# Kernel optimization log

Measured on AMD Instinct MI355X. Metric: run time of the kernel, lower is better.

## Reference

```python
import jax, jax.numpy as jnp
import numpy as np

LN_EPS = 1e-5

def layernorm(x, g, b):
    mu = jnp.mean(x, axis=-1, keepdims=True)
    var = jnp.mean(jnp.square(x - mu), axis=-1, keepdims=True)
    return (x - mu) * jax.lax.rsqrt(var + LN_EPS) * g + b

def setup_inputs() -> dict:
    B, T, C, H = 4, 1024, 1024, 16
    hd = C // H
    key = jax.random.key(0)
    ks = jax.random.split(key, 16)
    s = 0.02
    inp = {
        "x":  jax.random.normal(ks[0], (B, T, C), jnp.float32),
        # per-head QKV projections, stacked over heads: [H, C, hd] / [H, hd]
        "Wq": jax.random.normal(ks[1], (H, C, hd), jnp.float32) * s,
        "bq": jax.random.normal(ks[2], (H, hd), jnp.float32) * s,
        "Wk": jax.random.normal(ks[3], (H, C, hd), jnp.float32) * s,
        "bk": jax.random.normal(ks[4], (H, hd), jnp.float32) * s,
        "Wv": jax.random.normal(ks[5], (H, C, hd), jnp.float32) * s,
        "bv": jax.random.normal(ks[6], (H, hd), jnp.float32) * s,
        # LayerNorm params: ln1, ln2 (decoder), lnf (inside FeedForward)
        "g1": 1.0 + jax.random.normal(ks[7], (C,), jnp.float32) * s,
        "b1": jax.random.normal(ks[8], (C,), jnp.float32) * s,
        "g2": 1.0 + jax.random.normal(ks[9], (C,), jnp.float32) * s,
        "b2": jax.random.normal(ks[10], (C,), jnp.float32) * s,
        "gf": 1.0 + jax.random.normal(ks[11], (C,), jnp.float32) * s,
        "bf": jax.random.normal(ks[12], (C,), jnp.float32) * s,
        # FFN
        "W1": jax.random.normal(ks[13], (C, 4 * C), jnp.float32) * s,
        "b1f": jnp.zeros((4 * C,), jnp.float32),
        "W2": jax.random.normal(ks[14], (4 * C, C), jnp.float32) * s,
        "b2f": jnp.zeros((C,), jnp.float32),
    }
    return inp

def reference(x, Wq, bq, Wk, bk, Wv, bv, g1, b1, g2, b2, gf, bf, W1, b1f, W2, b2f):
    B, T, C = x.shape
    h = layernorm(x, g1, b1)                      # ln1
    # multi-head causal attention (per-head projections stacked on H)
    q = jnp.einsum("btc,hcd->bhtd", h, Wq) + bq[None, :, None, :]
    k = jnp.einsum("btc,hcd->bhtd", h, Wk) + bk[None, :, None, :]
    v = jnp.einsum("btc,hcd->bhtd", h, Wv) + bv[None, :, None, :]
    # NOTE: original scales by C**-0.5 (n_embd), not head_size**-0.5
    att = jnp.einsum("bhtd,bhsd->bhts", q, k) / jnp.sqrt(jnp.float32(C))
    causal = jnp.tril(jnp.ones((T, T), bool))
    att = jnp.where(causal, att, -jnp.inf)
    att = jax.nn.softmax(att, axis=-1)
    o = jnp.einsum("bhts,bhsd->bhtd", att, v)     # [B,H,T,hd]
    o = jnp.transpose(o, (0, 2, 1, 3)).reshape(B, T, C)  # concat heads
    x2 = h + o
    x3 = layernorm(x2, g2, b2)                    # ln2
    # FeedForward: hf = ln(x3); out = net(hf) + hf  (residual uses post-LN!)
    hf = layernorm(x3, gf, bf)
    ff = jax.nn.relu(hf @ W1 + b1f) @ W2 + b2f + hf
    return x3 + ff                                # dropout is identity in eval
```

## Files before the change

### kernel.cpp

```cpp
#include <hip/hip_runtime.h>
#include <hip/hip_bf16.h>


typedef __attribute__((ext_vector_type(8))) short short8;
typedef __attribute__((ext_vector_type(4))) short short4v;
typedef __attribute__((ext_vector_type(4))) float f32x4;

#define DEVI static __device__ __forceinline__

#define BAR() __builtin_amdgcn_s_barrier()
#define SB0() __builtin_amdgcn_sched_barrier(0)
#define LGKM0()                                         \
  {                                                     \
    asm volatile("s_waitcnt lgkmcnt(0)" ::: "memory");  \
    __builtin_amdgcn_sched_barrier(0);                  \
  }
#define VMW(n)                                              \
  {                                                         \
    asm volatile("s_waitcnt vmcnt(" #n ")" ::: "memory");   \
    __builtin_amdgcn_sched_barrier(0);                      \
  }

DEVI void gload_lds16(const void* g, void* l) {
  __builtin_amdgcn_global_load_lds(
      (const __attribute__((address_space(1))) void*)g,
      (__attribute__((address_space(3))) void*)l, 16, 0, 0);
}

DEVI float bf2f(short s) {
  union { float f; unsigned u; } cv;
  cv.u = ((unsigned)(unsigned short)s) << 16;
  return cv.f;
}
DEVI short f2bf(float f) {
  union { float f; unsigned u; } cv;
  cv.f = f;
  unsigned u = cv.u;
  u += 0x7FFFu + ((u >> 16) & 1u);
  return (short)(u >> 16);
}

DEVI void block_reduce2(float& s, float& s2, float* red, int t) {
#pragma unroll
  for (int off = 1; off < 64; off <<= 1) {
    s += __shfl_xor(s, off, 64);
    s2 += __shfl_xor(s2, off, 64);
  }
  __syncthreads();
  if ((t & 63) == 0) { red[(t >> 6) * 2] = s; red[(t >> 6) * 2 + 1] = s2; }
  __syncthreads();
  s = red[0] + red[2] + red[4] + red[6];
  s2 = red[1] + red[3] + red[5] + red[7];
}

DEVI void xcd_swz(int gx, int gy, int& bx, int& by) {
  const int flat = blockIdx.y * gx + blockIdx.x;
  const int c = (gx * gy) >> 3;
  const int nf = (flat & 7) * c + (flat >> 3);
  bx = nf % gx;
  by = nf / gx;
}

__global__ __launch_bounds__(256) void transpose_to_bf16(
    const float* __restrict__ in, short* __restrict__ out, int R, int C) {
  __shared__ float tile[32][33];
  const int b = blockIdx.z;
  in += (size_t)b * R * C;
  out += (size_t)b * R * C;
  const int r0 = blockIdx.y * 32, c0 = blockIdx.x * 32;
  const int tx = threadIdx.x, ty = threadIdx.y;
#pragma unroll
  for (int i = 0; i < 32; i += 8)
    tile[ty + i][tx] = in[(size_t)(r0 + ty + i) * C + c0 + tx];
  __syncthreads();
#pragma unroll
  for (int i = 0; i < 32; i += 8)
    out[(size_t)(c0 + ty + i) * R + r0 + tx] = f2bf(tile[tx][ty + i]);
}

__global__ __launch_bounds__(256) void transpose_qkv(
    const float* __restrict__ Wq, const float* __restrict__ Wk,
    const float* __restrict__ Wv, short* __restrict__ out) {
  __shared__ float tile[32][33];
  const int z = blockIdx.z;
  const int sel = z >> 4, b = z & 15;
  const float* in = (sel == 0) ? Wq : (sel == 1) ? Wk : Wv;
  in += (size_t)b * 1024 * 64;
  short* o = out + (size_t)sel * 1024 * 1024 + (size_t)b * 1024 * 64;
  const int r0 = blockIdx.y * 32, c0 = blockIdx.x * 32;
  const int tx = threadIdx.x, ty = threadIdx.y;
#pragma unroll
  for (int i = 0; i < 32; i += 8)
    tile[ty + i][tx] = in[(size_t)(r0 + ty + i) * 64 + c0 + tx];
  __syncthreads();
#pragma unroll
  for (int i = 0; i < 32; i += 8)
    o[(size_t)(c0 + ty + i) * 1024 + r0 + tx] = f2bf(tile[tx][ty + i]);
}

__global__ __launch_bounds__(256) void ln1_kernel(
    const float* __restrict__ x, const float* __restrict__ g,
    const float* __restrict__ b, float* __restrict__ hf,
    short* __restrict__ hb) {
  __shared__ float red[8];
  const int row = blockIdx.x, t = threadIdx.x;
  float4 v = ((const float4*)(x + (size_t)row * 1024))[t];
  float s = v.x + v.y + v.z + v.w;
  float s2 = v.x * v.x + v.y * v.y + v.z * v.z + v.w * v.w;
  block_reduce2(s, s2, red, t);
  const float mu = s * (1.0f / 1024.0f);
  const float rstd = rsqrtf(s2 * (1.0f / 1024.0f) - mu * mu + 1e-5f);
  float4 gv = ((const float4*)g)[t], bv = ((const float4*)b)[t];
  float4 o;
  o.x = (v.x - mu) * rstd * gv.x + bv.x;
  o.y = (v.y - mu) * rstd * gv.y + bv.y;
  o.z = (v.z - mu) * rstd * gv.z + bv.z;
  o.w = (v.w - mu) * rstd * gv.w + bv.w;
  ((float4*)(hf + (size_t)row * 1024))[t] = o;
  short4v p = {f2bf(o.x), f2bf(o.y), f2bf(o.z), f2bf(o.w)};
  ((short4v*)(hb + (size_t)row * 1024))[t] = p;
}

__global__ __launch_bounds__(256) void ln2f_kernel(
    const float* __restrict__ h, const float* __restrict__ o,
    const float* __restrict__ g2, const float* __restrict__ b2,
    const float* __restrict__ gf, const float* __restrict__ bfp,
    float* __restrict__ x3, short* __restrict__ hfb) {
  __shared__ float red[8];
  const int row = blockIdx.x, t = threadIdx.x;
  float4 hv = ((const float4*)(h + (size_t)row * 1024))[t];
  float4 ov = ((const float4*)(o + (size_t)row * 1024))[t];
  float4 v;
  v.x = hv.x + ov.x; v.y = hv.y + ov.y; v.z = hv.z + ov.z; v.w = hv.w + ov.w;
  float s = v.x + v.y + v.z + v.w;
  float s2 = v.x * v.x + v.y * v.y + v.z * v.z + v.w * v.w;
  block_reduce2(s, s2, red, t);
  float mu = s * (1.0f / 1024.0f);
  float rstd = rsqrtf(s2 * (1.0f / 1024.0f) - mu * mu + 1e-5f);
  float4 gv = ((const float4*)g2)[t], bv = ((const float4*)b2)[t];
  float4 xv;
  xv.x = (v.x - mu) * rstd * gv.x + bv.x;
  xv.y = (v.y - mu) * rstd * gv.y + bv.y;
  xv.z = (v.z - mu) * rstd * gv.z + bv.z;
  xv.w = (v.w - mu) * rstd * gv.w + bv.w;
  ((float4*)(x3 + (size_t)row * 1024))[t] = xv;
  s = xv.x + xv.y + xv.z + xv.w;
  s2 = xv.x * xv.x + xv.y * xv.y + xv.z * xv.z + xv.w * xv.w;
  block_reduce2(s, s2, red, t);
  mu = s * (1.0f / 1024.0f);
  rstd = rsqrtf(s2 * (1.0f / 1024.0f) - mu * mu + 1e-5f);
  float4 gv2 = ((const float4*)gf)[t], bv2 = ((const float4*)bfp)[t];
  short4v pk = {f2bf((xv.x - mu) * rstd * gv2.x + bv2.x),
                f2bf((xv.y - mu) * rstd * gv2.y + bv2.y),
                f2bf((xv.z - mu) * rstd * gv2.z + bv2.z),
                f2bf((xv.w - mu) * rstd * gv2.w + bv2.w)};
  ((short4v*)(hfb + (size_t)row * 1024))[t] = pk;
}

template <int EPI>
DEVI void gemm8_body(const short* __restrict__ A, const short* __restrict__ B,
                     int K, int kbase, int m0, int n0,
                     const float* __restrict__ f0, const float* __restrict__ f1,
                     const float* __restrict__ f2, short* __restrict__ s0,
                     short* __restrict__ s1, short* __restrict__ s2,
                     float* __restrict__ fo) {
  extern __shared__ __align__(16) char lds[];
  constexpr int NT = 16;
  const int tid = threadIdx.x;
  const int l = tid & 63, w = tid >> 6;
  const int wrM = w >> 2, wcN = w & 3;
  const int lr = l & 15, lg = l >> 4;

  const int cswz = (((lr & 1) << 2) | lg) ^ (lr >> 1);
  const int laneoff = ((lr >> 1) << 7) + (cswz << 4);

  const int rsel = l >> 3;
  const int scz = (l & 7) ^ rsel;
  const int s_roff = w * 16 + rsel * 2 + (scz >> 2);
  const int s_kc = (scz & 3) * 8;
  const short* Asrc = A + (size_t)(m0 + s_roff) * K + kbase + s_kc;
  const short* Bsrc = B + (size_t)(n0 + s_roff) * K + kbase + s_kc;
  const size_t rstep = (size_t)128 * K;

  auto STAGE = [&](int op, int kh, int t) {
    const short* g = (op ? Bsrc : Asrc) + t * 64 + kh * 32;
    char* d = lds + ((t & 1) * 65536 + op * 32768 + kh * 16384 + w * 1024);
    gload_lds16(g, d);
    gload_lds16(g + rstep, d + 8192);
  };

  f32x4 acc[8][4] = {};

  STAGE(0, 0, 0); STAGE(1, 0, 0); STAGE(0, 1, 0); STAGE(1, 1, 0);
  VMW(4); BAR(); SB0();

  for (int t = 0; t < NT; ++t) {
    const char* pa = lds + (t & 1) * 65536 + wrM * 8192 + laneoff;
    const char* pb = lds + (t & 1) * 65536 + 32768 + wcN * 4096 + laneoff;
    const bool st = (t + 1) < NT;
    short8 a[8], b[4];

#pragma unroll
    for (int mt = 0; mt < 8; ++mt) a[mt] = *(const short8*)(pa + mt * 1024);
#pragma unroll
    for (int nt = 0; nt < 4; ++nt) b[nt] = *(const short8*)(pb + nt * 1024);
    if (st) STAGE(0, 0, t + 1);
    BAR(); LGKM0();
    __builtin_amdgcn_s_setprio(1);
#pragma unroll
    for (int mt = 0; mt < 8; ++mt) {
      acc[mt][0] = __builtin_amdgcn_mfma_f32_16x16x32_bf16(a[mt], b[0], acc[mt][0], 0, 0, 0);
      acc[mt][1] = __builtin_amdgcn_mfma_f32_16x16x32_bf16(a[mt], b[1], acc[mt][1], 0, 0, 0);
    }
    __builtin_amdgcn_s_setprio(0);
    BAR(); SB0();

    if (st) STAGE(1, 0, t + 1);
    BAR(); SB0();
    __builtin_amdgcn_s_setprio(1);
#pragma unroll
    for (int mt = 0; mt < 8; ++mt) {
      acc[mt][2] = __builtin_amdgcn_mfma_f32_16x16x32_bf16(a[mt], b[2], acc[mt][2], 0, 0, 0);
      acc[mt][3] = __builtin_amdgcn_mfma_f32_16x16x32_bf16(a[mt], b[3], acc[mt][3], 0, 0, 0);
    }
    __builtin_amdgcn_s_setprio(0);
    if (st) { VMW(4); } else { VMW(0); }
    BAR(); SB0();

    pa += 16384; pb += 16384;
#pragma unroll
    for (int mt = 0; mt < 8; ++mt) a[mt] = *(const short8*)(pa + mt * 1024);
#pragma unroll
    for (int nt = 0; nt < 4; ++nt) b[nt] = *(const short8*)(pb + nt * 1024);
    if (st) STAGE(0, 1, t + 1);
    BAR(); LGKM0();
    __builtin_amdgcn_s_setprio(1);
#pragma unroll
    for (int mt = 0; mt < 8; ++mt) {
      acc[mt][0] = __builtin_amdgcn_mfma_f32_16x16x32_bf16(a[mt], b[0], acc[mt][0], 0, 0, 0);
      acc[mt][1] = __builtin_amdgcn_mfma_f32_16x16x32_bf16(a[mt], b[1], acc[mt][1], 0, 0, 0);
    }
    __builtin_amdgcn_s_setprio(0);
    BAR(); SB0();

    if (st) STAGE(1, 1, t + 1);
    BAR(); SB0();
    __builtin_amdgcn_s_setprio(1);
#pragma unroll
    for (int mt = 0; mt < 8; ++mt) {
      acc[mt][2] = __builtin_amdgcn_mfma_f32_16x16x32_bf16(a[mt], b[2], acc[mt][2], 0, 0, 0);
      acc[mt][3] = __builtin_amdgcn_mfma_f32_16x16x32_bf16(a[mt], b[3], acc[mt][3], 0, 0, 0);
    }
    __builtin_amdgcn_s_setprio(0);
    if (st) VMW(4);
    BAR(); SB0();
  }

#pragma unroll
  for (int mt = 0; mt < 8; ++mt) {
#pragma unroll
    for (int nt = 0; nt < 4; ++nt) {
      const int col = n0 + wcN * 64 + nt * 16 + lr;
      const int row0 = m0 + wrM * 128 + mt * 16 + lg * 4;
      if constexpr (EPI == 0) {
        const int sel = col >> 10, nn = col & 1023;
        const int hh = nn >> 6, dd = nn & 63;
        const int bb = row0 >> 10, tt0 = row0 & 1023;
        if (sel == 2) {
          const float bias = f2[nn];
          short4v pk = {f2bf(acc[mt][nt][0] + bias), f2bf(acc[mt][nt][1] + bias),
                        f2bf(acc[mt][nt][2] + bias), f2bf(acc[mt][nt][3] + bias)};
          *(short4v*)&s2[(((size_t)(bb * 16 + hh)) * 64 + dd) * 1024 + tt0] = pk;
        } else {
          const float bias = (sel == 0) ? f0[nn] : f1[nn];
          short* dst = (sel == 0) ? s0 : s1;
#pragma unroll
          for (int r = 0; r < 4; ++r)
            dst[(((size_t)(bb * 16 + hh)) * 1024 + tt0 + r) * 64 + dd] =
                f2bf(acc[mt][nt][r] + bias);
        }
      } else if constexpr (EPI == 1) {
#pragma unroll
        for (int r = 0; r < 4; ++r) {
          float val = fmaxf(acc[mt][nt][r] + f0[col], 0.0f);
          s0[(size_t)(row0 + r) * 4096 + col] = f2bf(val);
        }
      } else {
#pragma unroll
        for (int r = 0; r < 4; ++r)
          fo[(size_t)(row0 + r) * 1024 + col] = acc[mt][nt][r];
      }
    }
  }
}

__global__ __launch_bounds__(512, 2) void gemm8_qkv(
    const short* __restrict__ A, const short* __restrict__ B,
    const float* __restrict__ bq, const float* __restrict__ bk,
    const float* __restrict__ bv, short* __restrict__ q,
    short* __restrict__ k, short* __restrict__ vt) {
  int bx, by;
  xcd_swz(12, 16, bx, by);
  gemm8_body<0>(A, B, 1024, 0, by * 256, bx * 256, bq, bk, bv,
                q, k, vt, nullptr);
}

__global__ __launch_bounds__(512, 2) void gemm8_ffn1(
    const short* __restrict__ A, const short* __restrict__ B,
    const float* __restrict__ b1f, short* __restrict__ u) {
  int bx, by;
  xcd_swz(16, 16, bx, by);
  gemm8_body<1>(A, B, 1024, 0, by * 256, bx * 256, b1f,
                nullptr, nullptr, u, nullptr, nullptr, nullptr);
}

__global__ __launch_bounds__(512, 2) void gemm8_ffn2sk(
    const short* __restrict__ A, const short* __restrict__ B,
    float* __restrict__ part) {
  const int z = blockIdx.z;
  int bx, by;
  xcd_swz(4, 16, bx, by);
  gemm8_body<2>(A, B, 4096, z * 1024, by * 256, bx * 256,
                nullptr, nullptr, nullptr, nullptr, nullptr, nullptr,
                part + (size_t)z * 4096 * 1024);
}

__global__ __launch_bounds__(256) void ffn2_reduce(
    const float* __restrict__ part, const float* __restrict__ b2f,
    const short* __restrict__ hfb, const float* __restrict__ x3,
    float* __restrict__ out) {
  const size_t i = (size_t)blockIdx.x * 256 + threadIdx.x;
  const size_t S = (size_t)4096 * 1024 / 4;
  float4 a0 = ((const float4*)part)[i];
  float4 a1 = ((const float4*)part)[i + S];
  float4 a2 = ((const float4*)part)[i + 2 * S];
  float4 a3 = ((const float4*)part)[i + 3 * S];
  float4 bb = ((const float4*)b2f)[i & 255];
  float4 xv = ((const float4*)x3)[i];
  short4v hv = ((const short4v*)hfb)[i];
  float4 o;
  o.x = a0.x + a1.x + a2.x + a3.x + bb.x + bf2f(hv.x) + xv.x;
  o.y = a0.y + a1.y + a2.y + a3.y + bb.y + bf2f(hv.y) + xv.y;
  o.z = a0.z + a1.z + a2.z + a3.z + bb.z + bf2f(hv.z) + xv.z;
  o.w = a0.w + a1.w + a2.w + a3.w + bb.w + bf2f(hv.w) + xv.w;
  ((float4*)out)[i] = o;
}

__global__ __launch_bounds__(256, 5) void attn_kernel(
    const short* __restrict__ q, const short* __restrict__ k,
    const short* __restrict__ vt, float* __restrict__ o) {
  __shared__ __align__(16) short Ksm[64 * 64];
  __shared__ __align__(16) short Vsm[64 * 64];
  __shared__ __align__(16) short Psm[4 * 16 * 64];
  const int bh = blockIdx.x;
  const int qt = 15 - blockIdx.y;
  const int tid = threadIdx.x, lane = tid & 63, w = tid >> 6;
  const int lr = lane & 15, lg = lane >> 4;

  const short* qb = q + (size_t)bh * 1024 * 64;
  const short* kb = k + (size_t)bh * 1024 * 64;
  const short* vb = vt + (size_t)bh * 64 * 1024;

  const int qrow = qt * 64 + w * 16 + lr;
  short8 qf0 = *(const short8*)&qb[(size_t)qrow * 64 + lg * 8];
  short8 qf1 = *(const short8*)&qb[(size_t)qrow * 64 + 32 + lg * 8];

  f32x4 oacc[4] = {};
  float mrun = -1e30f, lrun = 0.0f;

  const float scale2 = 0.03125f * 1.44269504088896f;
  const int srow = tid >> 3;
  const int sc8 = tid & 7;
  char* pw = (char*)(Psm + w * 1024);
  const int qloc = w * 16 + lr;
  const int rowswz = (lr & 7) << 4;

  short8 kreg[2], vreg[2];
#pragma unroll
  for (int p = 0; p < 2; ++p) {
    const int rr = srow + p * 32;
    kreg[p] = *(const short8*)&kb[(size_t)rr * 64 + sc8 * 8];
    vreg[p] = *(const short8*)&vb[(size_t)rr * 1024 + sc8 * 8];
  }

  for (int kt = 0; kt <= qt; ++kt) {
#pragma unroll
    for (int p = 0; p < 2; ++p) {
      const int rr = srow + p * 32;
      *(short8*)((char*)Ksm + rr * 128 + ((sc8 ^ (rr & 7)) << 4)) = kreg[p];
      *(short8*)((char*)Vsm + rr * 128 + ((sc8 ^ (rr & 7)) << 4)) = vreg[p];
    }
    __syncthreads();
    if (kt < qt) {
#pragma unroll
      for (int p = 0; p < 2; ++p) {
        const int rr = srow + p * 32;
        kreg[p] =
            *(const short8*)&kb[((size_t)((kt + 1) * 64 + rr)) * 64 + sc8 * 8];
        vreg[p] =
            *(const short8*)&vb[(size_t)rr * 1024 + (kt + 1) * 64 + sc8 * 8];
      }
    }

    f32x4 sfr[4];
#pragma unroll
    for (int nt = 0; nt < 4; ++nt) {
      const int krow = nt * 16 + lr;
      short8 kf0 = *(const short8*)((const char*)Ksm + krow * 128 +
                                    (((0 + lg) ^ (krow & 7)) << 4));
      short8 kf1 = *(const short8*)((const char*)Ksm + krow * 128 +
                                    (((4 + lg) ^ (krow & 7)) << 4));
      f32x4 z = {};
      z = __builtin_amdgcn_mfma_f32_16x16x32_bf16(kf0, qf0, z, 0, 0, 0);
      z = __builtin_amdgcn_mfma_f32_16x16x32_bf16(kf1, qf1, z, 0, 0, 0);
      sfr[nt] = z;
    }
    if (kt == qt) {
#pragma unroll
      for (int nt = 0; nt < 4; ++nt) {
        const int kb0 = nt * 16 + lg * 4;
#pragma unroll
        for (int r = 0; r < 4; ++r)
          sfr[nt][r] = (kb0 + r <= qloc) ? sfr[nt][r] * scale2 : -1e30f;
      }
    } else {
#pragma unroll
      for (int nt = 0; nt < 4; ++nt)
#pragma unroll
        for (int r = 0; r < 4; ++r) sfr[nt][r] *= scale2;
    }
    float pm;
    {
      float a0 = fmaxf(fmaxf(sfr[0][0], sfr[0][1]), fmaxf(sfr[0][2], sfr[0][3]));
      float a1 = fmaxf(fmaxf(sfr[1][0], sfr[1][1]), fmaxf(sfr[1][2], sfr[1][3]));
      float a2 = fmaxf(fmaxf(sfr[2][0], sfr[2][1]), fmaxf(sfr[2][2], sfr[2][3]));
      float a3 = fmaxf(fmaxf(sfr[3][0], sfr[3][1]), fmaxf(sfr[3][2], sfr[3][3]));
      pm = fmaxf(fmaxf(a0, a1), fmaxf(a2, a3));
      pm = fmaxf(pm, __shfl_xor(pm, 16, 64));
      pm = fmaxf(pm, __shfl_xor(pm, 32, 64));
    }
    if (!__all(pm - mrun <= 8.0f)) {
      const float mnew = fmaxf(mrun, pm);
      const float alpha = exp2f(mrun - mnew);
      mrun = mnew;
      lrun *= alpha;
#pragma unroll
      for (int nt = 0; nt < 4; ++nt)
#pragma unroll
        for (int r = 0; r < 4; ++r) oacc[nt][r] *= alpha;
    }
    float rs;
    {
#pragma unroll
      for (int nt = 0; nt < 4; ++nt)
#pragma unroll
        for (int r = 0; r < 4; ++r) sfr[nt][r] = exp2f(sfr[nt][r] - mrun);
      float s0 = (sfr[0][0] + sfr[0][1]) + (sfr[0][2] + sfr[0][3]);
      float s1 = (sfr[1][0] + sfr[1][1]) + (sfr[1][2] + sfr[1][3]);
      float s2 = (sfr[2][0] + sfr[2][1]) + (sfr[2][2] + sfr[2][3]);
      float s3 = (sfr[3][0] + sfr[3][1]) + (sfr[3][2] + sfr[3][3]);
      rs = (s0 + s1) + (s2 + s3);
      rs += __shfl_xor(rs, 16, 64);
      rs += __shfl_xor(rs, 32, 64);
    }
    lrun += rs;

#pragma unroll
    for (int nt = 0; nt < 4; ++nt) {
      unsigned w0, w1;
      asm("v_cvt_pk_bf16_f32 %0, %1, %2"
          : "=v"(w0) : "v"(sfr[nt][0]), "v"(sfr[nt][1]));
      asm("v_cvt_pk_bf16_f32 %0, %1, %2"
          : "=v"(w1) : "v"(sfr[nt][2]), "v"(sfr[nt][3]));
      uint2 pk2 = {w0, w1};
      *(uint2*)(pw + lr * 128 + ((nt * 32 + lg * 8) ^ rowswz)) = pk2;
    }

#pragma unroll
    for (int kc = 0; kc < 2; ++kc) {
      short8 pb8 = *(const short8*)(pw + lr * 128 + ((kc * 64 + lg * 16) ^ rowswz));
#pragma unroll
      for (int nt = 0; nt < 4; ++nt) {
        const int vrow = nt * 16 + lr;
        short8 vf = *(const short8*)((const char*)Vsm + vrow * 128 +
                                     (((kc * 4 + lg) ^ (vrow & 7)) << 4));
        oacc[nt] = __builtin_amdgcn_mfma_f32_16x16x32_bf16(vf, pb8, oacc[nt], 0, 0, 0);
      }
    }
    __syncthreads();
  }

  const float inv = 1.0f / lrun;
  float* ob = o + (size_t)(bh >> 4) * 1024 * 1024 +
              (size_t)(qt * 64 + qloc) * 1024 + (bh & 15) * 64;
#pragma unroll
  for (int nt = 0; nt < 4; ++nt) {
    float4 ov = {oacc[nt][0] * inv, oacc[nt][1] * inv, oacc[nt][2] * inv,
                 oacc[nt][3] * inv};
    *(float4*)&ob[nt * 16 + lg * 4] = ov;
  }
}

extern "C" void kernel_launch(void* const* d_in, const int* in_sizes, int n_in,
                              void* d_out, int out_size, void* d_ws,
                              size_t ws_size, hipStream_t stream) {
  const float* x = (const float*)d_in[0];
  const float* Wq = (const float*)d_in[1];
  const float* bq = (const float*)d_in[2];
  const float* Wk = (const float*)d_in[3];
  const float* bk = (const float*)d_in[4];
  const float* Wv = (const float*)d_in[5];
  const float* bv = (const float*)d_in[6];
  const float* g1 = (const float*)d_in[7];
  const float* b1 = (const float*)d_in[8];
  const float* g2 = (const float*)d_in[9];
  const float* b2 = (const float*)d_in[10];
  const float* gf = (const float*)d_in[11];
  const float* bfp = (const float*)d_in[12];
  const float* W1 = (const float*)d_in[13];
  const float* b1f = (const float*)d_in[14];
  const float* W2 = (const float*)d_in[15];
  const float* b2f = (const float*)d_in[16];
  float* out = (float*)d_out;

  hipFuncSetAttribute((const void*)gemm8_qkv,
                      hipFuncAttributeMaxDynamicSharedMemorySize, 131072);
  hipFuncSetAttribute((const void*)gemm8_ffn1,
                      hipFuncAttributeMaxDynamicSharedMemorySize, 131072);
  hipFuncSetAttribute((const void*)gemm8_ffn2sk,
                      hipFuncAttributeMaxDynamicSharedMemorySize, 131072);

  const size_t MB = 1024 * 1024;
  char* p = (char*)d_ws;
  float* hbuf = (float*)(p + 0 * MB);
  short* qbuf = (short*)(p + 16 * MB);
  short* kbuf = (short*)(p + 24 * MB);
  short* vtb = (short*)(p + 32 * MB);
  float* obuf = (float*)(p + 40 * MB);
  short* wqkv_t = (short*)(p + 56 * MB);
  short* w1_t = (short*)(p + 62 * MB);
  float* part = (float*)(p + 0 * MB);
  char* q = p + 70 * MB;
  short* w2_t = (short*)(q + 0 * MB);
  short* hbb = (short*)(q + 8 * MB);
  float* x3b = (float*)(q + 16 * MB);
  short* hfb = (short*)(q + 32 * MB);
  short* ub = (short*)(q + 40 * MB);

  dim3 tb(32, 8);
  transpose_qkv<<<dim3(2, 32, 48), tb, 0, stream>>>(Wq, Wk, Wv, wqkv_t);
  transpose_to_bf16<<<dim3(128, 32, 1), tb, 0, stream>>>(W1, w1_t, 1024, 4096);
  transpose_to_bf16<<<dim3(32, 128, 1), tb, 0, stream>>>(W2, w2_t, 4096, 1024);

  ln1_kernel<<<4096, 256, 0, stream>>>(x, g1, b1, hbuf, hbb);

  gemm8_qkv<<<dim3(12, 16), 512, 131072, stream>>>(hbb, wqkv_t, bq, bk, bv,
                                                   qbuf, kbuf, vtb);

  attn_kernel<<<dim3(64, 16), 256, 0, stream>>>(qbuf, kbuf, vtb, obuf);

  ln2f_kernel<<<4096, 256, 0, stream>>>(hbuf, obuf, g2, b2, gf, bfp, x3b, hfb);

  gemm8_ffn1<<<dim3(16, 16), 512, 131072, stream>>>(hfb, w1_t, b1f, ub);

  gemm8_ffn2sk<<<dim3(4, 16, 4), 512, 131072, stream>>>(ub, w2_t, part);

  ffn2_reduce<<<4096, 256, 0, stream>>>(part, b2f, hfb, x3b, out);
}
```

Baseline: 195.9 us.

## Shrink GEMM tiles to 128x128 with 4 waves and halve split-K

```diff
diff --git a/kernel.cpp b/kernel.cpp
--- a/kernel.cpp
+++ b/kernel.cpp
@@ -158,17 +158,16 @@
 }
 
 template <int EPI>
-DEVI void gemm8_body(const short* __restrict__ A, const short* __restrict__ B,
-                     int K, int kbase, int m0, int n0,
+DEVI void gemm4_body(const short* __restrict__ A, const short* __restrict__ B,
+                     int K, int kbase, int ktiles, int m0, int n0,
                      const float* __restrict__ f0, const float* __restrict__ f1,
                      const float* __restrict__ f2, short* __restrict__ s0,
                      short* __restrict__ s1, short* __restrict__ s2,
                      float* __restrict__ fo) {
   extern __shared__ __align__(16) char lds[];
-  constexpr int NT = 16;
   const int tid = threadIdx.x;
   const int l = tid & 63, w = tid >> 6;
-  const int wrM = w >> 2, wcN = w & 3;
+  const int wrM = w >> 1, wcN = w & 1;
   const int lr = l & 15, lg = l >> 4;
 
   const int cswz = (((lr & 1) << 2) | lg) ^ (lr >> 1);
@@ -180,88 +179,53 @@
   const int s_kc = (scz & 3) * 8;
   const short* Asrc = A + (size_t)(m0 + s_roff) * K + kbase + s_kc;
   const short* Bsrc = B + (size_t)(n0 + s_roff) * K + kbase + s_kc;
-  const size_t rstep = (size_t)128 * K;
+  const size_t rstep = (size_t)64 * K;
 
   auto STAGE = [&](int op, int kh, int t) {
     const short* g = (op ? Bsrc : Asrc) + t * 64 + kh * 32;
-    char* d = lds + ((t & 1) * 65536 + op * 32768 + kh * 16384 + w * 1024);
+    char* d = lds + ((t & 1) * 32768 + op * 16384 + kh * 8192 + w * 1024);
     gload_lds16(g, d);
-    gload_lds16(g + rstep, d + 8192);
+    gload_lds16(g + rstep, d + 4096);
   };
 
-  f32x4 acc[8][4] = {};
+  f32x4 acc[4][4] = {};
 
   STAGE(0, 0, 0); STAGE(1, 0, 0); STAGE(0, 1, 0); STAGE(1, 1, 0);
   VMW(4); BAR(); SB0();
 
-  for (int t = 0; t < NT; ++t) {
-    const char* pa = lds + (t & 1) * 65536 + wrM * 8192 + laneoff;
-    const char* pb = lds + (t & 1) * 65536 + 32768 + wcN * 4096 + laneoff;
-    const bool st = (t + 1) < NT;
-    short8 a[8], b[4];
-
-#pragma unroll
-    for (int mt = 0; mt < 8; ++mt) a[mt] = *(const short8*)(pa + mt * 1024);
-#pragma unroll
-    for (int nt = 0; nt < 4; ++nt) b[nt] = *(const short8*)(pb + nt * 1024);
-    if (st) STAGE(0, 0, t + 1);
-    BAR(); LGKM0();
-    __builtin_amdgcn_s_setprio(1);
-#pragma unroll
-    for (int mt = 0; mt < 8; ++mt) {
-      acc[mt][0] = __builtin_amdgcn_mfma_f32_16x16x32_bf16(a[mt], b[0], acc[mt][0], 0, 0, 0);
-      acc[mt][1] = __builtin_amdgcn_mfma_f32_16x16x32_bf16(a[mt], b[1], acc[mt][1], 0, 0, 0);
-    }
-    __builtin_amdgcn_s_setprio(0);
-    BAR(); SB0();
-
-    if (st) STAGE(1, 0, t + 1);
-    BAR(); SB0();
-    __builtin_amdgcn_s_setprio(1);
-#pragma unroll
-    for (int mt = 0; mt < 8; ++mt) {
-      acc[mt][2] = __builtin_amdgcn_mfma_f32_16x16x32_bf16(a[mt], b[2], acc[mt][2], 0, 0, 0);
-      acc[mt][3] = __builtin_amdgcn_mfma_f32_16x16x32_bf16(a[mt], b[3], acc[mt][3], 0, 0, 0);
-    }
-    __builtin_amdgcn_s_setprio(0);
-    if (st) { VMW(4); } else { VMW(0); }
-    BAR(); SB0();
-
-    pa += 16384; pb += 16384;
-#pragma unroll
-    for (int mt = 0; mt < 8; ++mt) a[mt] = *(const short8*)(pa + mt * 1024);
-#pragma unroll
-    for (int nt = 0; nt < 4; ++nt) b[nt] = *(const short8*)(pb + nt * 1024);
-    if (st) STAGE(0, 1, t + 1);
-    BAR(); LGKM0();
-    __builtin_amdgcn_s_setprio(1);
-#pragma unroll
-    for (int mt = 0; mt < 8; ++mt) {
-      acc[mt][0] = __builtin_amdgcn_mfma_f32_16x16x32_bf16(a[mt], b[0], acc[mt][0], 0, 0, 0);
-      acc[mt][1] = __builtin_amdgcn_mfma_f32_16x16x32_bf16(a[mt], b[1], acc[mt][1], 0, 0, 0);
-    }
-    __builtin_amdgcn_s_setprio(0);
-    BAR(); SB0();
-
-    if (st) STAGE(1, 1, t + 1);
-    BAR(); SB0();
-    __builtin_amdgcn_s_setprio(1);
-#pragma unroll
-    for (int mt = 0; mt < 8; ++mt) {
-      acc[mt][2] = __builtin_amdgcn_mfma_f32_16x16x32_bf16(a[mt], b[2], acc[mt][2], 0, 0, 0);
-      acc[mt][3] = __builtin_amdgcn_mfma_f32_16x16x32_bf16(a[mt], b[3], acc[mt][3], 0, 0, 0);
-    }
-    __builtin_amdgcn_s_setprio(0);
-    if (st) VMW(4);
-    BAR(); SB0();
-  }
-
-#pragma unroll
-  for (int mt = 0; mt < 8; ++mt) {
+  for (int t = 0; t < ktiles; ++t) {
+    const bool st = (t + 1) < ktiles;
+#pragma unroll
+    for (int kh = 0; kh < 2; ++kh) {
+      const char* pa = lds + (t & 1) * 32768 + kh * 8192 + wrM * 4096 + laneoff;
+      const char* pb =
+          lds + (t & 1) * 32768 + 16384 + kh * 8192 + wcN * 4096 + laneoff;
+      short8 a[4], b[4];
+#pragma unroll
+      for (int mt = 0; mt < 4; ++mt) a[mt] = *(const short8*)(pa + mt * 1024);
+#pragma unroll
+      for (int nt = 0; nt < 4; ++nt) b[nt] = *(const short8*)(pb + nt * 1024);
+      if (st) { STAGE(0, kh, t + 1); STAGE(1, kh, t + 1); }
+      LGKM0();
+      __builtin_amdgcn_s_setprio(1);
+#pragma unroll
+      for (int mt = 0; mt < 4; ++mt)
+#pragma unroll
+        for (int nt = 0; nt < 4; ++nt)
+          acc[mt][nt] = __builtin_amdgcn_mfma_f32_16x16x32_bf16(
+              a[mt], b[nt], acc[mt][nt], 0, 0, 0);
+      __builtin_amdgcn_s_setprio(0);
+      if (st) { VMW(4); } else if (kh == 0) { VMW(0); }
+      BAR(); SB0();
+    }
+  }
+
+#pragma unroll
+  for (int mt = 0; mt < 4; ++mt) {
 #pragma unroll
     for (int nt = 0; nt < 4; ++nt) {
       const int col = n0 + wcN * 64 + nt * 16 + lr;
-      const int row0 = m0 + wrM * 128 + mt * 16 + lg * 4;
+      const int row0 = m0 + wrM * 64 + mt * 16 + lg * 4;
       if constexpr (EPI == 0) {
         const int sel = col >> 10, nn = col & 1023;
         const int hh = nn >> 6, dd = nn & 63;
@@ -294,34 +258,34 @@
   }
 }
 
-__global__ __launch_bounds__(512, 2) void gemm8_qkv(
+__global__ __launch_bounds__(256, 2) void gemm4_qkv(
     const short* __restrict__ A, const short* __restrict__ B,
     const float* __restrict__ bq, const float* __restrict__ bk,
     const float* __restrict__ bv, short* __restrict__ q,
     short* __restrict__ k, short* __restrict__ vt) {
   int bx, by;
-  xcd_swz(12, 16, bx, by);
-  gemm8_body<0>(A, B, 1024, 0, by * 256, bx * 256, bq, bk, bv,
-                q, k, vt, nullptr);
-}
-
-__global__ __launch_bounds__(512, 2) void gemm8_ffn1(
+  xcd_swz(24, 32, bx, by);
+  gemm4_body<0>(A, B, 1024, 0, 16, by * 128, bx * 128, bq, bk, bv, q, k, vt,
+                nullptr);
+}
+
+__global__ __launch_bounds__(256, 2) void gemm4_ffn1(
     const short* __restrict__ A, const short* __restrict__ B,
     const float* __restrict__ b1f, short* __restrict__ u) {
   int bx, by;
-  xcd_swz(16, 16, bx, by);
-  gemm8_body<1>(A, B, 1024, 0, by * 256, bx * 256, b1f,
-                nullptr, nullptr, u, nullptr, nullptr, nullptr);
-}
-
-__global__ __launch_bounds__(512, 2) void gemm8_ffn2sk(
+  xcd_swz(32, 32, bx, by);
+  gemm4_body<1>(A, B, 1024, 0, 16, by * 128, bx * 128, b1f, nullptr, nullptr,
+                u, nullptr, nullptr, nullptr);
+}
+
+__global__ __launch_bounds__(256, 2) void gemm4_ffn2sk(
     const short* __restrict__ A, const short* __restrict__ B,
     float* __restrict__ part) {
   const int z = blockIdx.z;
   int bx, by;
-  xcd_swz(4, 16, bx, by);
-  gemm8_body<2>(A, B, 4096, z * 1024, by * 256, bx * 256,
-                nullptr, nullptr, nullptr, nullptr, nullptr, nullptr,
+  xcd_swz(8, 32, bx, by);
+  gemm4_body<2>(A, B, 4096, z * 2048, 32, by * 128, bx * 128, nullptr, nullptr,
+                nullptr, nullptr, nullptr, nullptr,
                 part + (size_t)z * 4096 * 1024);
 }
 
@@ -333,16 +297,14 @@
   const size_t S = (size_t)4096 * 1024 / 4;
   float4 a0 = ((const float4*)part)[i];
   float4 a1 = ((const float4*)part)[i + S];
-  float4 a2 = ((const float4*)part)[i + 2 * S];
-  float4 a3 = ((const float4*)part)[i + 3 * S];
   float4 bb = ((const float4*)b2f)[i & 255];
   float4 xv = ((const float4*)x3)[i];
   short4v hv = ((const short4v*)hfb)[i];
   float4 o;
-  o.x = a0.x + a1.x + a2.x + a3.x + bb.x + bf2f(hv.x) + xv.x;
-  o.y = a0.y + a1.y + a2.y + a3.y + bb.y + bf2f(hv.y) + xv.y;
-  o.z = a0.z + a1.z + a2.z + a3.z + bb.z + bf2f(hv.z) + xv.z;
-  o.w = a0.w + a1.w + a2.w + a3.w + bb.w + bf2f(hv.w) + xv.w;
+  o.x = a0.x + a1.x + bb.x + bf2f(hv.x) + xv.x;
+  o.y = a0.y + a1.y + bb.y + bf2f(hv.y) + xv.y;
+  o.z = a0.z + a1.z + bb.z + bf2f(hv.z) + xv.z;
+  o.w = a0.w + a1.w + bb.w + bf2f(hv.w) + xv.w;
   ((float4*)out)[i] = o;
 }
 
@@ -523,12 +485,12 @@
   const float* b2f = (const float*)d_in[16];
   float* out = (float*)d_out;
 
-  hipFuncSetAttribute((const void*)gemm8_qkv,
-                      hipFuncAttributeMaxDynamicSharedMemorySize, 131072);
-  hipFuncSetAttribute((const void*)gemm8_ffn1,
-                      hipFuncAttributeMaxDynamicSharedMemorySize, 131072);
-  hipFuncSetAttribute((const void*)gemm8_ffn2sk,
-                      hipFuncAttributeMaxDynamicSharedMemorySize, 131072);
+  hipFuncSetAttribute((const void*)gemm4_qkv,
+                      hipFuncAttributeMaxDynamicSharedMemorySize, 65536);
+  hipFuncSetAttribute((const void*)gemm4_ffn1,
+                      hipFuncAttributeMaxDynamicSharedMemorySize, 65536);
+  hipFuncSetAttribute((const void*)gemm4_ffn2sk,
+                      hipFuncAttributeMaxDynamicSharedMemorySize, 65536);
 
   const size_t MB = 1024 * 1024;
   char* p = (char*)d_ws;
@@ -554,16 +516,16 @@
 
   ln1_kernel<<<4096, 256, 0, stream>>>(x, g1, b1, hbuf, hbb);
 
-  gemm8_qkv<<<dim3(12, 16), 512, 131072, stream>>>(hbb, wqkv_t, bq, bk, bv,
-                                                   qbuf, kbuf, vtb);
+  gemm4_qkv<<<dim3(24, 32), 256, 65536, stream>>>(hbb, wqkv_t, bq, bk, bv,
+                                                  qbuf, kbuf, vtb);
 
   attn_kernel<<<dim3(64, 16), 256, 0, stream>>>(qbuf, kbuf, vtb, obuf);
 
   ln2f_kernel<<<4096, 256, 0, stream>>>(hbuf, obuf, g2, b2, gf, bfp, x3b, hfb);
 
-  gemm8_ffn1<<<dim3(16, 16), 512, 131072, stream>>>(hfb, w1_t, b1f, ub);
-
-  gemm8_ffn2sk<<<dim3(4, 16, 4), 512, 131072, stream>>>(ub, w2_t, part);
+  gemm4_ffn1<<<dim3(32, 32), 256, 65536, stream>>>(hfb, w1_t, b1f, ub);
+
+  gemm4_ffn2sk<<<dim3(8, 32, 2), 256, 65536, stream>>>(ub, w2_t, part);
 
   ffn2_reduce<<<4096, 256, 0, stream>>>(part, b2f, hfb, x3b, out);
 }
```

Result: slower. 199.9 us (+2.1%).

## Deepen GEMM LDS pipeline to four 32-wide K stages with prefetch distance three

Applied to the files above, without the earlier changes.

```diff
diff --git a/kernel.cpp b/kernel.cpp
--- a/kernel.cpp
+++ b/kernel.cpp
@@ -165,7 +165,7 @@
                      short* __restrict__ s1, short* __restrict__ s2,
                      float* __restrict__ fo) {
   extern __shared__ __align__(16) char lds[];
-  constexpr int NT = 16;
+  constexpr int NT = 32;
   const int tid = threadIdx.x;
   const int l = tid & 63, w = tid >> 6;
   const int wrM = w >> 2, wcN = w & 3;
@@ -182,29 +182,30 @@
   const short* Bsrc = B + (size_t)(n0 + s_roff) * K + kbase + s_kc;
   const size_t rstep = (size_t)128 * K;
 
-  auto STAGE = [&](int op, int kh, int t) {
-    const short* g = (op ? Bsrc : Asrc) + t * 64 + kh * 32;
-    char* d = lds + ((t & 1) * 65536 + op * 32768 + kh * 16384 + w * 1024);
+  auto STAGE = [&](int op, int t) {
+    const short* g = (op ? Bsrc : Asrc) + t * 32;
+    char* d = lds + ((t & 3) * 32768 + op * 16384 + w * 1024);
     gload_lds16(g, d);
     gload_lds16(g + rstep, d + 8192);
   };
 
   f32x4 acc[8][4] = {};
 
-  STAGE(0, 0, 0); STAGE(1, 0, 0); STAGE(0, 1, 0); STAGE(1, 1, 0);
-  VMW(4); BAR(); SB0();
+  STAGE(0, 0); STAGE(1, 0); STAGE(0, 1); STAGE(1, 1); STAGE(0, 2); STAGE(1, 2);
+  VMW(8); BAR(); SB0();
 
   for (int t = 0; t < NT; ++t) {
-    const char* pa = lds + (t & 1) * 65536 + wrM * 8192 + laneoff;
-    const char* pb = lds + (t & 1) * 65536 + 32768 + wcN * 4096 + laneoff;
-    const bool st = (t + 1) < NT;
+    const char* base = lds + (t & 3) * 32768;
+    const char* pa = base + wrM * 8192 + laneoff;
+    const char* pb = base + 16384 + wcN * 4096 + laneoff;
+    const bool st = (t + 3) < NT;
     short8 a[8], b[4];
 
 #pragma unroll
     for (int mt = 0; mt < 8; ++mt) a[mt] = *(const short8*)(pa + mt * 1024);
-#pragma unroll
-    for (int nt = 0; nt < 4; ++nt) b[nt] = *(const short8*)(pb + nt * 1024);
-    if (st) STAGE(0, 0, t + 1);
+    b[0] = *(const short8*)(pb);
+    b[1] = *(const short8*)(pb + 1024);
+    if (st) STAGE(0, t + 3);
     BAR(); LGKM0();
     __builtin_amdgcn_s_setprio(1);
 #pragma unroll
@@ -215,8 +216,10 @@
     __builtin_amdgcn_s_setprio(0);
     BAR(); SB0();
 
-    if (st) STAGE(1, 0, t + 1);
-    BAR(); SB0();
+    b[2] = *(const short8*)(pb + 2048);
+    b[3] = *(const short8*)(pb + 3072);
+    if (st) STAGE(1, t + 3);
+    BAR(); LGKM0();
     __builtin_amdgcn_s_setprio(1);
 #pragma unroll
     for (int mt = 0; mt < 8; ++mt) {
@@ -224,35 +227,9 @@
       acc[mt][3] = __builtin_amdgcn_mfma_f32_16x16x32_bf16(a[mt], b[3], acc[mt][3], 0, 0, 0);
     }
     __builtin_amdgcn_s_setprio(0);
-    if (st) { VMW(4); } else { VMW(0); }
-    BAR(); SB0();
-
-    pa += 16384; pb += 16384;
-#pragma unroll
-    for (int mt = 0; mt < 8; ++mt) a[mt] = *(const short8*)(pa + mt * 1024);
-#pragma unroll
-    for (int nt = 0; nt < 4; ++nt) b[nt] = *(const short8*)(pb + nt * 1024);
-    if (st) STAGE(0, 1, t + 1);
-    BAR(); LGKM0();
-    __builtin_amdgcn_s_setprio(1);
-#pragma unroll
-    for (int mt = 0; mt < 8; ++mt) {
-      acc[mt][0] = __builtin_amdgcn_mfma_f32_16x16x32_bf16(a[mt], b[0], acc[mt][0], 0, 0, 0);
-      acc[mt][1] = __builtin_amdgcn_mfma_f32_16x16x32_bf16(a[mt], b[1], acc[mt][1], 0, 0, 0);
-    }
-    __builtin_amdgcn_s_setprio(0);
-    BAR(); SB0();
-
-    if (st) STAGE(1, 1, t + 1);
-    BAR(); SB0();
-    __builtin_amdgcn_s_setprio(1);
-#pragma unroll
-    for (int mt = 0; mt < 8; ++mt) {
-      acc[mt][2] = __builtin_amdgcn_mfma_f32_16x16x32_bf16(a[mt], b[2], acc[mt][2], 0, 0, 0);
-      acc[mt][3] = __builtin_amdgcn_mfma_f32_16x16x32_bf16(a[mt], b[3], acc[mt][3], 0, 0, 0);
-    }
-    __builtin_amdgcn_s_setprio(0);
-    if (st) VMW(4);
+    if ((t + 3) < NT) { VMW(8); }
+    else if ((t + 2) < NT) { VMW(4); }
+    else if ((t + 1) < NT) { VMW(0); }
     BAR(); SB0();
   }
 
@@ -301,8 +278,8 @@
     short* __restrict__ k, short* __restrict__ vt) {
   int bx, by;
   xcd_swz(12, 16, bx, by);
-  gemm8_body<0>(A, B, 1024, 0, by * 256, bx * 256, bq, bk, bv,
-                q, k, vt, nullptr);
+  gemm8_body<0>(A, B, 1024, 0, by * 256, bx * 256, bq, bk, bv, q, k, vt,
+                nullptr);
 }
 
 __global__ __launch_bounds__(512, 2) void gemm8_ffn1(
@@ -310,8 +287,8 @@
     const float* __restrict__ b1f, short* __restrict__ u) {
   int bx, by;
   xcd_swz(16, 16, bx, by);
-  gemm8_body<1>(A, B, 1024, 0, by * 256, bx * 256, b1f,
-                nullptr, nullptr, u, nullptr, nullptr, nullptr);
+  gemm8_body<1>(A, B, 1024, 0, by * 256, bx * 256, b1f, nullptr, nullptr, u,
+                nullptr, nullptr, nullptr);
 }
 
 __global__ __launch_bounds__(512, 2) void gemm8_ffn2sk(
@@ -320,8 +297,8 @@
   const int z = blockIdx.z;
   int bx, by;
   xcd_swz(4, 16, bx, by);
-  gemm8_body<2>(A, B, 4096, z * 1024, by * 256, bx * 256,
-                nullptr, nullptr, nullptr, nullptr, nullptr, nullptr,
+  gemm8_body<2>(A, B, 4096, z * 1024, by * 256, bx * 256, nullptr, nullptr,
+                nullptr, nullptr, nullptr, nullptr,
                 part + (size_t)z * 4096 * 1024);
 }
 
```

After: 202.0 us. 1.03x slower.

## Store intermediate activations and split-K partials in bf16 instead of fp32

Applied to the files above, without the earlier changes.

```diff
diff --git a/kernel.cpp b/kernel.cpp
--- a/kernel.cpp
+++ b/kernel.cpp
@@ -100,8 +100,7 @@
 
 __global__ __launch_bounds__(256) void ln1_kernel(
     const float* __restrict__ x, const float* __restrict__ g,
-    const float* __restrict__ b, float* __restrict__ hf,
-    short* __restrict__ hb) {
+    const float* __restrict__ b, short* __restrict__ hb) {
   __shared__ float red[8];
   const int row = blockIdx.x, t = threadIdx.x;
   float4 v = ((const float4*)(x + (size_t)row * 1024))[t];
@@ -111,27 +110,27 @@
   const float mu = s * (1.0f / 1024.0f);
   const float rstd = rsqrtf(s2 * (1.0f / 1024.0f) - mu * mu + 1e-5f);
   float4 gv = ((const float4*)g)[t], bv = ((const float4*)b)[t];
-  float4 o;
-  o.x = (v.x - mu) * rstd * gv.x + bv.x;
-  o.y = (v.y - mu) * rstd * gv.y + bv.y;
-  o.z = (v.z - mu) * rstd * gv.z + bv.z;
-  o.w = (v.w - mu) * rstd * gv.w + bv.w;
-  ((float4*)(hf + (size_t)row * 1024))[t] = o;
-  short4v p = {f2bf(o.x), f2bf(o.y), f2bf(o.z), f2bf(o.w)};
+  short4v p = {f2bf((v.x - mu) * rstd * gv.x + bv.x),
+               f2bf((v.y - mu) * rstd * gv.y + bv.y),
+               f2bf((v.z - mu) * rstd * gv.z + bv.z),
+               f2bf((v.w - mu) * rstd * gv.w + bv.w)};
   ((short4v*)(hb + (size_t)row * 1024))[t] = p;
 }
 
 __global__ __launch_bounds__(256) void ln2f_kernel(
-    const float* __restrict__ h, const float* __restrict__ o,
+    const short* __restrict__ hbb, const short* __restrict__ ob,
     const float* __restrict__ g2, const float* __restrict__ b2,
     const float* __restrict__ gf, const float* __restrict__ bfp,
-    float* __restrict__ x3, short* __restrict__ hfb) {
+    short* __restrict__ x3, short* __restrict__ hfb) {
   __shared__ float red[8];
   const int row = blockIdx.x, t = threadIdx.x;
-  float4 hv = ((const float4*)(h + (size_t)row * 1024))[t];
-  float4 ov = ((const float4*)(o + (size_t)row * 1024))[t];
+  short4v hv4 = ((const short4v*)(hbb + (size_t)row * 1024))[t];
+  short4v ov4 = ((const short4v*)(ob + (size_t)row * 1024))[t];
   float4 v;
-  v.x = hv.x + ov.x; v.y = hv.y + ov.y; v.z = hv.z + ov.z; v.w = hv.w + ov.w;
+  v.x = bf2f(hv4.x) + bf2f(ov4.x);
+  v.y = bf2f(hv4.y) + bf2f(ov4.y);
+  v.z = bf2f(hv4.z) + bf2f(ov4.z);
+  v.w = bf2f(hv4.w) + bf2f(ov4.w);
   float s = v.x + v.y + v.z + v.w;
   float s2 = v.x * v.x + v.y * v.y + v.z * v.z + v.w * v.w;
   block_reduce2(s, s2, red, t);
@@ -143,7 +142,8 @@
   xv.y = (v.y - mu) * rstd * gv.y + bv.y;
   xv.z = (v.z - mu) * rstd * gv.z + bv.z;
   xv.w = (v.w - mu) * rstd * gv.w + bv.w;
-  ((float4*)(x3 + (size_t)row * 1024))[t] = xv;
+  short4v xp = {f2bf(xv.x), f2bf(xv.y), f2bf(xv.z), f2bf(xv.w)};
+  ((short4v*)(x3 + (size_t)row * 1024))[t] = xp;
   s = xv.x + xv.y + xv.z + xv.w;
   s2 = xv.x * xv.x + xv.y * xv.y + xv.z * xv.z + xv.w * xv.w;
   block_reduce2(s, s2, red, t);
@@ -162,8 +162,7 @@
                      int K, int kbase, int m0, int n0,
                      const float* __restrict__ f0, const float* __restrict__ f1,
                      const float* __restrict__ f2, short* __restrict__ s0,
-                     short* __restrict__ s1, short* __restrict__ s2,
-                     float* __restrict__ fo) {
+                     short* __restrict__ s1, short* __restrict__ s2) {
   extern __shared__ __align__(16) char lds[];
   constexpr int NT = 16;
   const int tid = threadIdx.x;
@@ -288,7 +287,7 @@
       } else {
 #pragma unroll
         for (int r = 0; r < 4; ++r)
-          fo[(size_t)(row0 + r) * 1024 + col] = acc[mt][nt][r];
+          s0[(size_t)(row0 + r) * 1024 + col] = f2bf(acc[mt][nt][r]);
       }
     }
   }
@@ -301,8 +300,7 @@
     short* __restrict__ k, short* __restrict__ vt) {
   int bx, by;
   xcd_swz(12, 16, bx, by);
-  gemm8_body<0>(A, B, 1024, 0, by * 256, bx * 256, bq, bk, bv,
-                q, k, vt, nullptr);
+  gemm8_body<0>(A, B, 1024, 0, by * 256, bx * 256, bq, bk, bv, q, k, vt);
 }
 
 __global__ __launch_bounds__(512, 2) void gemm8_ffn1(
@@ -310,45 +308,44 @@
     const float* __restrict__ b1f, short* __restrict__ u) {
   int bx, by;
   xcd_swz(16, 16, bx, by);
-  gemm8_body<1>(A, B, 1024, 0, by * 256, bx * 256, b1f,
-                nullptr, nullptr, u, nullptr, nullptr, nullptr);
+  gemm8_body<1>(A, B, 1024, 0, by * 256, bx * 256, b1f, nullptr, nullptr, u,
+                nullptr, nullptr);
 }
 
 __global__ __launch_bounds__(512, 2) void gemm8_ffn2sk(
     const short* __restrict__ A, const short* __restrict__ B,
-    float* __restrict__ part) {
+    short* __restrict__ part) {
   const int z = blockIdx.z;
   int bx, by;
   xcd_swz(4, 16, bx, by);
-  gemm8_body<2>(A, B, 4096, z * 1024, by * 256, bx * 256,
-                nullptr, nullptr, nullptr, nullptr, nullptr, nullptr,
-                part + (size_t)z * 4096 * 1024);
+  gemm8_body<2>(A, B, 4096, z * 1024, by * 256, bx * 256, nullptr, nullptr,
+                nullptr, part + (size_t)z * 4096 * 1024, nullptr, nullptr);
 }
 
 __global__ __launch_bounds__(256) void ffn2_reduce(
-    const float* __restrict__ part, const float* __restrict__ b2f,
-    const short* __restrict__ hfb, const float* __restrict__ x3,
+    const short* __restrict__ part, const float* __restrict__ b2f,
+    const short* __restrict__ hfb, const short* __restrict__ x3,
     float* __restrict__ out) {
   const size_t i = (size_t)blockIdx.x * 256 + threadIdx.x;
   const size_t S = (size_t)4096 * 1024 / 4;
-  float4 a0 = ((const float4*)part)[i];
-  float4 a1 = ((const float4*)part)[i + S];
-  float4 a2 = ((const float4*)part)[i + 2 * S];
-  float4 a3 = ((const float4*)part)[i + 3 * S];
+  short4v a0 = ((const short4v*)part)[i];
+  short4v a1 = ((const short4v*)part)[i + S];
+  short4v a2 = ((const short4v*)part)[i + 2 * S];
+  short4v a3 = ((const short4v*)part)[i + 3 * S];
   float4 bb = ((const float4*)b2f)[i & 255];
-  float4 xv = ((const float4*)x3)[i];
+  short4v xv = ((const short4v*)x3)[i];
   short4v hv = ((const short4v*)hfb)[i];
   float4 o;
-  o.x = a0.x + a1.x + a2.x + a3.x + bb.x + bf2f(hv.x) + xv.x;
-  o.y = a0.y + a1.y + a2.y + a3.y + bb.y + bf2f(hv.y) + xv.y;
-  o.z = a0.z + a1.z + a2.z + a3.z + bb.z + bf2f(hv.z) + xv.z;
-  o.w = a0.w + a1.w + a2.w + a3.w + bb.w + bf2f(hv.w) + xv.w;
+  o.x = bf2f(a0.x) + bf2f(a1.x) + bf2f(a2.x) + bf2f(a3.x) + bb.x + bf2f(hv.x) + bf2f(xv.x);
+  o.y = bf2f(a0.y) + bf2f(a1.y) + bf2f(a2.y) + bf2f(a3.y) + bb.y + bf2f(hv.y) + bf2f(xv.y);
+  o.z = bf2f(a0.z) + bf2f(a1.z) + bf2f(a2.z) + bf2f(a3.z) + bb.z + bf2f(hv.z) + bf2f(xv.z);
+  o.w = bf2f(a0.w) + bf2f(a1.w) + bf2f(a2.w) + bf2f(a3.w) + bb.w + bf2f(hv.w) + bf2f(xv.w);
   ((float4*)out)[i] = o;
 }
 
 __global__ __launch_bounds__(256, 5) void attn_kernel(
     const short* __restrict__ q, const short* __restrict__ k,
-    const short* __restrict__ vt, float* __restrict__ o) {
+    const short* __restrict__ vt, short* __restrict__ o) {
   __shared__ __align__(16) short Ksm[64 * 64];
   __shared__ __align__(16) short Vsm[64 * 64];
   __shared__ __align__(16) short Psm[4 * 16 * 64];
@@ -491,13 +488,13 @@
   }
 
   const float inv = 1.0f / lrun;
-  float* ob = o + (size_t)(bh >> 4) * 1024 * 1024 +
+  short* ob = o + (size_t)(bh >> 4) * 1024 * 1024 +
               (size_t)(qt * 64 + qloc) * 1024 + (bh & 15) * 64;
 #pragma unroll
   for (int nt = 0; nt < 4; ++nt) {
-    float4 ov = {oacc[nt][0] * inv, oacc[nt][1] * inv, oacc[nt][2] * inv,
-                 oacc[nt][3] * inv};
-    *(float4*)&ob[nt * 16 + lg * 4] = ov;
+    short4v pk = {f2bf(oacc[nt][0] * inv), f2bf(oacc[nt][1] * inv),
+                  f2bf(oacc[nt][2] * inv), f2bf(oacc[nt][3] * inv)};
+    *(short4v*)&ob[nt * 16 + lg * 4] = pk;
   }
 }
 
@@ -532,34 +529,33 @@
 
   const size_t MB = 1024 * 1024;
   char* p = (char*)d_ws;
-  float* hbuf = (float*)(p + 0 * MB);
-  short* qbuf = (short*)(p + 16 * MB);
-  short* kbuf = (short*)(p + 24 * MB);
-  short* vtb = (short*)(p + 32 * MB);
-  float* obuf = (float*)(p + 40 * MB);
-  short* wqkv_t = (short*)(p + 56 * MB);
-  short* w1_t = (short*)(p + 62 * MB);
-  float* part = (float*)(p + 0 * MB);
-  char* q = p + 70 * MB;
+  short* qbuf = (short*)(p + 0 * MB);
+  short* kbuf = (short*)(p + 8 * MB);
+  short* vtb = (short*)(p + 16 * MB);
+  short* obuf = (short*)(p + 24 * MB);
+  short* wqkv_t = (short*)(p + 32 * MB);
+  short* w1_t = (short*)(p + 40 * MB);
+  short* part = (short*)(p + 0 * MB);
+  char* q = p + 48 * MB;
   short* w2_t = (short*)(q + 0 * MB);
   short* hbb = (short*)(q + 8 * MB);
-  float* x3b = (float*)(q + 16 * MB);
-  short* hfb = (short*)(q + 32 * MB);
-  short* ub = (short*)(q + 40 * MB);
+  short* x3b = (short*)(q + 16 * MB);
+  short* hfb = (short*)(q + 24 * MB);
+  short* ub = (short*)(q + 32 * MB);
 
   dim3 tb(32, 8);
   transpose_qkv<<<dim3(2, 32, 48), tb, 0, stream>>>(Wq, Wk, Wv, wqkv_t);
   transpose_to_bf16<<<dim3(128, 32, 1), tb, 0, stream>>>(W1, w1_t, 1024, 4096);
   transpose_to_bf16<<<dim3(32, 128, 1), tb, 0, stream>>>(W2, w2_t, 4096, 1024);
 
-  ln1_kernel<<<4096, 256, 0, stream>>>(x, g1, b1, hbuf, hbb);
+  ln1_kernel<<<4096, 256, 0, stream>>>(x, g1, b1, hbb);
 
   gemm8_qkv<<<dim3(12, 16), 512, 131072, stream>>>(hbb, wqkv_t, bq, bk, bv,
                                                    qbuf, kbuf, vtb);
 
   attn_kernel<<<dim3(64, 16), 256, 0, stream>>>(qbuf, kbuf, vtb, obuf);
 
-  ln2f_kernel<<<4096, 256, 0, stream>>>(hbuf, obuf, g2, b2, gf, bfp, x3b, hfb);
+  ln2f_kernel<<<4096, 256, 0, stream>>>(hbb, obuf, g2, b2, gf, bfp, x3b, hfb);
 
   gemm8_ffn1<<<dim3(16, 16), 512, 131072, stream>>>(hfb, w1_t, b1f, ub);
 
```

Measured after the change: 182.0 us. 1.08x faster.
